# Kernel optimization log

Hardware: AMD Instinct MI355X
Metric: run time of the kernel (lower is better)

Reference implementation:

```python
import jax, jax.numpy as jnp
import numpy as np

D_MODEL = 1024
NHEAD = 16
HEAD_DIM = D_MODEL // NHEAD
B, L = 4, 4096
LN_EPS = 1e-5


def setup_inputs() -> dict:
    key = jax.random.key(0)
    ks = jax.random.split(key, 8)
    x = jax.random.normal(ks[0], (B, L, D_MODEL), dtype=jnp.float32)
    sin = jnp.zeros((L, HEAD_DIM), dtype=jnp.float32)
    cos = jnp.zeros((L, HEAD_DIM), dtype=jnp.float32)
    # decay[:,1,0] is read as per-head lambda in (0,1)
    decay = jax.random.uniform(ks[1], (NHEAD, 2, 1), dtype=jnp.float32)
    scale = 0.02
    Wq = jax.random.normal(ks[2], (D_MODEL, D_MODEL), dtype=jnp.float32) * scale
    Wv = jax.random.normal(ks[3], (D_MODEL, D_MODEL), dtype=jnp.float32) * scale
    Wo = jax.random.normal(ks[4], (D_MODEL, D_MODEL), dtype=jnp.float32) * scale
    Wg = jax.random.normal(ks[5], (D_MODEL, D_MODEL), dtype=jnp.float32) * scale
    ln_g = jnp.ones((D_MODEL,), dtype=jnp.float32)
    ln_b = jnp.zeros((D_MODEL,), dtype=jnp.float32)
    return {"x": x, "sin": sin, "cos": cos, "decay": decay,
            "Wq": Wq, "Wv": Wv, "Wo": Wo, "Wg": Wg,
            "ln_g": ln_g, "ln_b": ln_b}


def _retention(v, lam):
    # v: [B,L,H,Dh], lam: [H] -> cumulative decayed sum over L
    def step(state, v_t):  # state,[B,H,Dh]
        state = lam[None, :, None] * state + v_t
        return state, state
    v_l_first = jnp.swapaxes(v, 0, 1)  # [L,B,H,Dh]
    init = jnp.zeros(v_l_first.shape[1:], dtype=v.dtype)
    _, states = jax.lax.scan(step, init, v_l_first)
    return jnp.swapaxes(states, 0, 1)  # [B,L,H,Dh]


def reference(x, sin, cos, decay, Wq, Wv, Wo, Wg, ln_g, ln_b):
    del sin, cos  # discarded by the module
    Bx, Lx, D = x.shape
    H = decay.shape[0]
    Dh = D // H
    q = (x @ Wq.T).reshape(Bx, Lx, H, Dh)
    v = (x @ Wv.T).reshape(Bx, Lx, H, Dh)
    lam = decay[:, 1, 0]  # [H]
    state = _retention(v, lam)  # [B,L,H,Dh]
    y = (q * state).reshape(Bx, Lx, D)
    # LayerNorm over last dim
    mu = jnp.mean(y, axis=-1, keepdims=True)
    var = jnp.mean(jnp.square(y - mu), axis=-1, keepdims=True)
    y = (y - mu) * jax.lax.rsqrt(var + LN_EPS) * ln_g + ln_b
    gate = jax.nn.silu(x @ Wg.T)
    y = y * gate
    return y @ Wo.T
```

## Files before the change

### kernel.cpp

```cpp
#include <hip/hip_runtime.h>

#define DM    1024
#define LSEQ  4096
#define BATCH 4
#define MROWS (BATCH * LSEQ)
#define MD    ((size_t)MROWS * DM)
#define DD    ((size_t)DM * DM)
#define CHUNK 32
#define NCH   (LSEQ / CHUNK)
#define NCHAIN (BATCH * DM)

typedef __attribute__((ext_vector_type(4))) float  f32x4;
typedef __attribute__((ext_vector_type(8))) __bf16 bf16x8;
typedef __attribute__((ext_vector_type(4))) __bf16 bf16x4;

__device__ __forceinline__ void gload_lds16(const void* g, void* l) {
  __builtin_amdgcn_global_load_lds(
      (const __attribute__((address_space(1))) void*)g,
      (__attribute__((address_space(3))) void*)l, 16, 0, 0);
}

__global__ __launch_bounds__(256) void cvt_bf16(const float* __restrict__ in,
                                                __bf16* __restrict__ out) {
  size_t i = ((size_t)blockIdx.x * 256 + threadIdx.x) * 4;
  f32x4 f = *(const f32x4*)(in + i);
  bf16x4 o;
#pragma unroll
  for (int j = 0; j < 4; ++j) o[j] = (__bf16)f[j];
  *(bf16x4*)(out + i) = o;
}


__device__ __forceinline__ int swz(int b) { return b ^ ((b >> 3) & 0x70); }

__device__ __forceinline__ bf16x8 ldf(const char* tile, int row, int k) {
  int lin = (row << 7) + (k << 1);
  return *(const bf16x8*)(tile + swz(lin));
}

__device__ __forceinline__ void stage_half(const __bf16* srcRow0, char* tile,
                                           int halfOff, int k0, int t) {
#pragma unroll
  for (int is = 0; is < 2; ++is) {
    int d = halfOff + is * 8192 + t * 16;
    int l = swz(d);
    int row = l >> 7, cb = l & 127;
    gload_lds16((const char*)srcRow0 + (size_t)row * (DM * 2) + k0 * 2 + cb,
                tile + d);
  }
}

template <typename OutT>
__global__ __launch_bounds__(512, 2) void gemm_nt(const __bf16* __restrict__ A,
                                                  const __bf16* __restrict__ Wb,
                                                  OutT* __restrict__ Cb) {
  constexpr int K = DM, N = DM, NT = K / 64;
  __shared__ __attribute__((aligned(128))) char lds[131072];

  const __bf16* Wp = Wb + (size_t)blockIdx.z * DD;
  OutT* Cp = Cb + (size_t)blockIdx.z * MD;

  const int orig = blockIdx.y * 4 + blockIdx.x;
  const int sid = (orig & 7) * 32 + (orig >> 3);
  const int bx = sid & 3, by = sid >> 2;
  const int m0 = by * 256, n0 = bx * 256;

  const int t = threadIdx.x, lane = t & 63, wv = t >> 6;
  const int wr = wv >> 2, wc = wv & 3;
  const int lrow = lane & 15, lk8 = (lane >> 4) * 8;

  const __bf16* Abase = A + (size_t)m0 * K;
  const __bf16* Bbase = Wp + (size_t)n0 * K;

  f32x4 acc[8][4] = {};
  bf16x8 a[4][2];
  bf16x8 bq[2][2][2];

  char* buf0 = lds;
  char* buf1 = lds + 65536;

  stage_half(Abase, buf0,         0,  0, t);
  stage_half(Abase, buf0,     16384,  0, t);
  stage_half(Bbase, buf0 + 32768, 0,  0, t);
  stage_half(Bbase, buf0 + 32768, 16384, 0, t);
  stage_half(Bbase, buf1 + 32768, 0, 64, t);
  stage_half(Abase, buf1,         0, 64, t);
  asm volatile("s_waitcnt vmcnt(4)" ::: "memory");
  __builtin_amdgcn_s_barrier();
  __builtin_amdgcn_sched_barrier(0);

#define LDA_(mh)                                                        \
  _Pragma("unroll") for (int mf = 0; mf < 4; ++mf)                      \
  _Pragma("unroll") for (int ks = 0; ks < 2; ++ks)                      \
    a[mf][ks] = ldf(At, wr * 128 + (mh) * 64 + mf * 16 + lrow, ks * 32 + lk8);
#define LDB_(nh)                                                        \
  _Pragma("unroll") for (int nf = 0; nf < 2; ++nf)                      \
  _Pragma("unroll") for (int ks = 0; ks < 2; ++ks)                      \
    bq[nh][nf][ks] = ldf(Bt, wc * 64 + (nh) * 32 + nf * 16 + lrow, ks * 32 + lk8);
#define MFMA16_(mh, nh)                                                 \
  __builtin_amdgcn_s_setprio(1);                                        \
  _Pragma("unroll") for (int mf = 0; mf < 4; ++mf)                      \
  _Pragma("unroll") for (int nf = 0; nf < 2; ++nf)                      \
  _Pragma("unroll") for (int ks = 0; ks < 2; ++ks)                      \
    acc[(mh) * 4 + mf][(nh) * 2 + nf] = __builtin_amdgcn_mfma_f32_16x16x32_bf16( \
        a[mf][ks], bq[nh][nf][ks], acc[(mh) * 4 + mf][(nh) * 2 + nf], 0, 0, 0); \
  __builtin_amdgcn_s_setprio(0);
#define SYNC_IN_                                                        \
  __builtin_amdgcn_s_barrier();                                         \
  asm volatile("s_waitcnt lgkmcnt(0)" ::: "memory");                    \
  __builtin_amdgcn_sched_barrier(0);
#define SYNC_OUT_                                                       \
  __builtin_amdgcn_s_barrier();                                         \
  __builtin_amdgcn_sched_barrier(0);

#pragma unroll 1
  for (int kt = 0; kt < NT; ++kt) {
    char* bufc = lds + (kt & 1) * 65536;
    char* bufn = lds + (((kt & 1) ^ 1)) * 65536;
    const char* At = bufc;
    const char* Bt = bufc + 32768;
    const int k1 = (kt + 1) << 6, k2 = (kt + 2) << 6;
    const bool s1 = (kt + 1 < NT), s2 = (kt + 2 < NT);

    LDA_(0); LDB_(0);
    if (s1) stage_half(Bbase, bufn + 32768, 16384, k1, t);
    SYNC_IN_; MFMA16_(0, 0); SYNC_OUT_;

    LDB_(1);
    if (s1) stage_half(Abase, bufn, 16384, k1, t);
    SYNC_IN_; MFMA16_(0, 1); SYNC_OUT_;

    LDA_(1);
    if (s2) stage_half(Bbase, bufc + 32768, 0, k2, t);
    SYNC_IN_; MFMA16_(1, 0); SYNC_OUT_;

    if (s2) stage_half(Abase, bufc, 0, k2, t);
    __builtin_amdgcn_s_barrier();
    __builtin_amdgcn_sched_barrier(0);
    MFMA16_(1, 1);
    if (s2) { asm volatile("s_waitcnt vmcnt(4)" ::: "memory"); }
    else    { asm volatile("s_waitcnt vmcnt(0)" ::: "memory"); }
    __builtin_amdgcn_s_barrier();
    __builtin_amdgcn_sched_barrier(0);
  }
#undef LDA_
#undef LDB_
#undef MFMA16_
#undef SYNC_IN_
#undef SYNC_OUT_

#pragma unroll
  for (int mi = 0; mi < 8; ++mi) {
    int r0 = m0 + wr * 128 + mi * 16 + (lane >> 4) * 4;
#pragma unroll
    for (int ni = 0; ni < 4; ++ni) {
      int c0 = n0 + wc * 64 + ni * 16 + (lane & 15);
#pragma unroll
      for (int j = 0; j < 4; ++j) {
        float v = acc[mi][ni][j];
        if constexpr (__is_same(OutT, float))
          Cp[(size_t)(r0 + j) * N + c0] = v;
        else
          Cp[(size_t)(r0 + j) * N + c0] = (__bf16)v;
      }
    }
  }
}

__global__ __launch_bounds__(256) void scan1(const __bf16* __restrict__ v,
                                             float* __restrict__ st,
                                             float* __restrict__ csum,
                                             const float* __restrict__ decay) {
  int tid = blockIdx.x * 256 + threadIdx.x;
  int dg = tid & 255;
  int b  = (tid >> 8) & 3;
  int c  = tid >> 10;
  int d0 = dg * 4;
  float lam = decay[((d0 >> 6) << 1) + 1];
  f32x4 s = {0.f, 0.f, 0.f, 0.f};
  size_t base = ((size_t)b * LSEQ + (size_t)c * CHUNK) * DM + d0;
  for (int t = 0; t < CHUNK; ++t) {
    bf16x4 vv = *(const bf16x4*)(v + base);
    f32x4 vf = {(float)vv[0], (float)vv[1], (float)vv[2], (float)vv[3]};
    s = lam * s + vf;
    *(f32x4*)(st + base) = s;
    base += DM;
  }
  *(f32x4*)(csum + (size_t)c * NCHAIN + b * DM + d0) = s;
}

__global__ __launch_bounds__(256) void scan2(const float* __restrict__ csum,
                                             float* __restrict__ carry,
                                             const float* __restrict__ decay) {
  int i = blockIdx.x * 256 + threadIdx.x;
  int ch0 = i * 4;
  int d0 = ch0 & (DM - 1);
  float lam = decay[((d0 >> 6) << 1) + 1];
  float l2 = lam * lam, l4 = l2 * l2, l8 = l4 * l4, l16 = l8 * l8;
  float lamC = l16 * l16;
  f32x4 cs = {0.f, 0.f, 0.f, 0.f};
  for (int c = 0; c < NCH; ++c) {
    *(f32x4*)(carry + (size_t)c * NCHAIN + ch0) = cs;
    f32x4 sm = *(const f32x4*)(csum + (size_t)c * NCHAIN + ch0);
    cs = lamC * cs + sm;
  }
}

__global__ __launch_bounds__(256) void fuse_ln(const __bf16* __restrict__ qb,
                                               const float* __restrict__ st,
                                               const float* __restrict__ carry,
                                               const __bf16* __restrict__ gb,
                                               const float* __restrict__ decay,
                                               const float* __restrict__ ln_g,
                                               const float* __restrict__ ln_b,
                                               __bf16* __restrict__ y2) {
  const int row = blockIdx.x;
  const int l = row & (LSEQ - 1), b = row >> 12;
  const int c = l >> 5, tl = l & (CHUNK - 1);
  const int d0 = threadIdx.x * 4;
  const float lam = decay[((d0 >> 6) << 1) + 1];
  const float p = __powf(lam, (float)(tl + 1));
  const size_t base = (size_t)row * DM + d0;

  f32x4 s4 = *(const f32x4*)(st + base);
  f32x4 cr = *(const f32x4*)(carry + (size_t)c * NCHAIN + b * DM + d0);
  bf16x4 q4 = *(const bf16x4*)(qb + base);

  f32x4 y;
  float sum = 0.f, ssq = 0.f;
#pragma unroll
  for (int i = 0; i < 4; ++i) {
    float yy = (float)q4[i] * (s4[i] + p * cr[i]);
    y[i] = yy;
    sum += yy;
    ssq += yy * yy;
  }
#pragma unroll
  for (int o = 32; o > 0; o >>= 1) {
    sum += __shfl_xor(sum, o);
    ssq += __shfl_xor(ssq, o);
  }
  __shared__ float sb[8];
  if ((threadIdx.x & 63) == 0) {
    sb[threadIdx.x >> 6] = sum;
    sb[4 + (threadIdx.x >> 6)] = ssq;
  }
  __syncthreads();
  sum = sb[0] + sb[1] + sb[2] + sb[3];
  ssq = sb[4] + sb[5] + sb[6] + sb[7];

  const float mu = sum * (1.0f / DM);
  const float var = ssq * (1.0f / DM) - mu * mu;
  const float rstd = rsqrtf(fmaxf(var, 0.0f) + 1e-5f);

  bf16x4 g4 = *(const bf16x4*)(gb + base);
  f32x4 lg = *(const f32x4*)(ln_g + d0);
  f32x4 lb = *(const f32x4*)(ln_b + d0);
  bf16x4 o4;
#pragma unroll
  for (int i = 0; i < 4; ++i) {
    float gv = (float)g4[i];
    float gate = gv / (1.0f + __expf(-gv));
    float val = fmaf((y[i] - mu) * rstd, lg[i], lb[i]) * gate;
    o4[i] = (__bf16)val;
  }
  *(bf16x4*)(y2 + base) = o4;
}

extern "C" void kernel_launch(void* const* d_in, const int* in_sizes, int n_in,
                              void* d_out, int out_size, void* d_ws, size_t ws_size,
                              hipStream_t stream) {
  const float* x     = (const float*)d_in[0];
  const float* decay = (const float*)d_in[3];
  const float* Wq    = (const float*)d_in[4];
  const float* Wv    = (const float*)d_in[5];
  const float* Wo    = (const float*)d_in[6];
  const float* Wg    = (const float*)d_in[7];
  const float* lng   = (const float*)d_in[8];
  const float* lnb   = (const float*)d_in[9];
  float* out = (float*)d_out;

  char* ws = (char*)d_ws;
  size_t off = 0;
  auto alloc = [&](size_t bytes) -> void* {
    void* p = ws + off;
    off += (bytes + 255) & ~(size_t)255;
    return p;
  };
  __bf16* xb   = (__bf16*)alloc(MD * 2);
  __bf16* wqvg = (__bf16*)alloc(3 * DD * 2);
  __bf16* wob  = (__bf16*)alloc(DD * 2);
  __bf16* qvg  = (__bf16*)alloc(3 * MD * 2);
  __bf16* y2b  = (__bf16*)alloc(MD * 2);
  float*  st   = (float*)alloc(MD * 4);
  float*  csum = (float*)alloc((size_t)NCH * NCHAIN * 4);
  float*  cry  = (float*)alloc((size_t)NCH * NCHAIN * 4);

  cvt_bf16<<<(int)(MD / 1024), 256, 0, stream>>>(x, xb);
  cvt_bf16<<<(int)(DD / 1024), 256, 0, stream>>>(Wq, wqvg);
  cvt_bf16<<<(int)(DD / 1024), 256, 0, stream>>>(Wv, wqvg + DD);
  cvt_bf16<<<(int)(DD / 1024), 256, 0, stream>>>(Wg, wqvg + 2 * DD);
  cvt_bf16<<<(int)(DD / 1024), 256, 0, stream>>>(Wo, wob);

  gemm_nt<__bf16><<<dim3(4, MROWS / 256, 3), 512, 0, stream>>>(xb, wqvg, qvg);

  scan1<<<(BATCH * NCH * (DM / 4)) / 256, 256, 0, stream>>>(qvg + MD, st, csum, decay);
  scan2<<<(NCHAIN / 4) / 256, 256, 0, stream>>>(csum, cry, decay);

  fuse_ln<<<MROWS, 256, 0, stream>>>(qvg, st, cry, qvg + 2 * MD, decay, lng, lnb, y2b);

  gemm_nt<float><<<dim3(4, MROWS / 256, 1), 512, 0, stream>>>(y2b, wob, out);
}
```

Baseline: 235.4 us.

## Restructure GEMM staging pipeline, recompute scan in fused LN kernel, batch weight casts

The GEMM's global-to-LDS staging now remaps tile rows so that each half-tile matches what the MFMA phases consume. Loads for tile k+2 are issued into the current buffer with vmcnt-based waits, and the accumulator-to-output mapping is updated to match. The first scan pass no longer writes the full fp32 state tensor. A new per-chunk kernel instead recomputes the within-chunk scan from v plus the carry, then applies LayerNorm and the SiLU gate over 32 rows, which removes a large fp32 write and read. The four weight casts are merged into one launch. The costs are higher register pressure (32 f32x4 kept live per thread), only 512 blocks in the fused kernel, and a more fragile wait-count schedule.

Result: faster. 215.5 us (-8.5%).

```diff
diff --git a/kernel.cpp b/kernel.cpp
--- a/kernel.cpp
+++ b/kernel.cpp
@@ -30,6 +30,21 @@
   *(bf16x4*)(out + i) = o;
 }
 
+__global__ __launch_bounds__(256) void cvt_w(const float* __restrict__ s0,
+                                             const float* __restrict__ s1,
+                                             const float* __restrict__ s2,
+                                             const float* __restrict__ s3,
+                                             __bf16* __restrict__ dst) {
+  const float* sp = (blockIdx.z == 0) ? s0 : (blockIdx.z == 1) ? s1
+                  : (blockIdx.z == 2) ? s2 : s3;
+  size_t i = ((size_t)blockIdx.x * 256 + threadIdx.x) * 4;
+  f32x4 f = *(const f32x4*)(sp + i);
+  bf16x4 o;
+#pragma unroll
+  for (int j = 0; j < 4; ++j) o[j] = (__bf16)f[j];
+  *(bf16x4*)(dst + (size_t)blockIdx.z * DD + i) = o;
+}
+
 
 __device__ __forceinline__ int swz(int b) { return b ^ ((b >> 3) & 0x70); }
 
@@ -38,15 +53,26 @@
   return *(const bf16x8*)(tile + swz(lin));
 }
 
-__device__ __forceinline__ void stage_half(const __bf16* srcRow0, char* tile,
-                                           int halfOff, int k0, int t) {
+__device__ __forceinline__ void stageA_half(const __bf16* Abase, char* tileA,
+                                            int h, int k0, int t) {
 #pragma unroll
   for (int is = 0; is < 2; ++is) {
-    int d = halfOff + is * 8192 + t * 16;
+    int d = h * 16384 + is * 8192 + t * 16;
     int l = swz(d);
-    int row = l >> 7, cb = l & 127;
-    gload_lds16((const char*)srcRow0 + (size_t)row * (DM * 2) + k0 * 2 + cb,
-                tile + d);
+    int lds_r = l >> 7, cb = l & 127;
+    int g = ((lds_r >> 6) & 1) * 128 + h * 64 + (lds_r & 63);
+    gload_lds16((const char*)Abase + (size_t)g * (DM * 2) + k0 * 2 + cb, tileA + d);
+  }
+}
+__device__ __forceinline__ void stageB_half(const __bf16* Bbase, char* tileB,
+                                            int h, int k0, int t) {
+#pragma unroll
+  for (int is = 0; is < 2; ++is) {
+    int d = h * 16384 + is * 8192 + t * 16;
+    int l = swz(d);
+    int lds_r = l >> 7, cb = l & 127;
+    int g = ((lds_r >> 5) & 3) * 64 + h * 32 + (lds_r & 31);
+    gload_lds16((const char*)Bbase + (size_t)g * (DM * 2) + k0 * 2 + cb, tileB + d);
   }
 }
 
@@ -79,24 +105,26 @@
   char* buf0 = lds;
   char* buf1 = lds + 65536;
 
-  stage_half(Abase, buf0,         0,  0, t);
-  stage_half(Abase, buf0,     16384,  0, t);
-  stage_half(Bbase, buf0 + 32768, 0,  0, t);
-  stage_half(Bbase, buf0 + 32768, 16384, 0, t);
-  stage_half(Bbase, buf1 + 32768, 0, 64, t);
-  stage_half(Abase, buf1,         0, 64, t);
-  asm volatile("s_waitcnt vmcnt(4)" ::: "memory");
+  stageA_half(Abase, buf0,         0, 0, t);
+  stageB_half(Bbase, buf0 + 32768, 0, 0, t);
+  stageB_half(Bbase, buf0 + 32768, 1, 0, t);
+  stageA_half(Abase, buf0,         1, 0, t);
+  stageA_half(Abase, buf1,         0, 64, t);
+  stageB_half(Bbase, buf1 + 32768, 0, 64, t);
+  stageB_half(Bbase, buf1 + 32768, 1, 64, t);
+  stageA_half(Abase, buf1,         1, 64, t);
+  asm volatile("s_waitcnt vmcnt(12)" ::: "memory");
   __builtin_amdgcn_s_barrier();
   __builtin_amdgcn_sched_barrier(0);
 
 #define LDA_(mh)                                                        \
   _Pragma("unroll") for (int mf = 0; mf < 4; ++mf)                      \
   _Pragma("unroll") for (int ks = 0; ks < 2; ++ks)                      \
-    a[mf][ks] = ldf(At, wr * 128 + (mh) * 64 + mf * 16 + lrow, ks * 32 + lk8);
+    a[mf][ks] = ldf(At, (mh) * 128 + wr * 64 + mf * 16 + lrow, ks * 32 + lk8);
 #define LDB_(nh)                                                        \
   _Pragma("unroll") for (int nf = 0; nf < 2; ++nf)                      \
   _Pragma("unroll") for (int ks = 0; ks < 2; ++ks)                      \
-    bq[nh][nf][ks] = ldf(Bt, wc * 64 + (nh) * 32 + nf * 16 + lrow, ks * 32 + lk8);
+    bq[nh][nf][ks] = ldf(Bt, (nh) * 128 + wc * 32 + nf * 16 + lrow, ks * 32 + lk8);
 #define MFMA16_(mh, nh)                                                 \
   __builtin_amdgcn_s_setprio(1);                                        \
   _Pragma("unroll") for (int mf = 0; mf < 4; ++mf)                      \
@@ -105,56 +133,54 @@
     acc[(mh) * 4 + mf][(nh) * 2 + nf] = __builtin_amdgcn_mfma_f32_16x16x32_bf16( \
         a[mf][ks], bq[nh][nf][ks], acc[(mh) * 4 + mf][(nh) * 2 + nf], 0, 0, 0); \
   __builtin_amdgcn_s_setprio(0);
-#define SYNC_IN_                                                        \
+#define BAR_LGKM_                                                       \
   __builtin_amdgcn_s_barrier();                                         \
   asm volatile("s_waitcnt lgkmcnt(0)" ::: "memory");                    \
   __builtin_amdgcn_sched_barrier(0);
-#define SYNC_OUT_                                                       \
+#define VM_BAR_(n)                                                      \
+  asm volatile("s_waitcnt vmcnt(" #n ")" ::: "memory");                 \
   __builtin_amdgcn_s_barrier();                                         \
   __builtin_amdgcn_sched_barrier(0);
 
 #pragma unroll 1
   for (int kt = 0; kt < NT; ++kt) {
     char* bufc = lds + (kt & 1) * 65536;
-    char* bufn = lds + (((kt & 1) ^ 1)) * 65536;
     const char* At = bufc;
     const char* Bt = bufc + 32768;
-    const int k1 = (kt + 1) << 6, k2 = (kt + 2) << 6;
-    const bool s1 = (kt + 1 < NT), s2 = (kt + 2 < NT);
+    const int k2 = ((kt + 2) & (NT - 1)) << 6;
 
     LDA_(0); LDB_(0);
-    if (s1) stage_half(Bbase, bufn + 32768, 16384, k1, t);
-    SYNC_IN_; MFMA16_(0, 0); SYNC_OUT_;
+    BAR_LGKM_; MFMA16_(0, 0);
+    VM_BAR_(10);
 
     LDB_(1);
-    if (s1) stage_half(Abase, bufn, 16384, k1, t);
-    SYNC_IN_; MFMA16_(0, 1); SYNC_OUT_;
+    stageA_half(Abase, bufc,         0, k2, t);
+    stageB_half(Bbase, bufc + 32768, 0, k2, t);
+    BAR_LGKM_; MFMA16_(0, 1);
+    VM_BAR_(12);
 
     LDA_(1);
-    if (s2) stage_half(Bbase, bufc + 32768, 0, k2, t);
-    SYNC_IN_; MFMA16_(1, 0); SYNC_OUT_;
-
-    if (s2) stage_half(Abase, bufc, 0, k2, t);
+    stageB_half(Bbase, bufc + 32768, 1, k2, t);
+    BAR_LGKM_; MFMA16_(1, 0);
     __builtin_amdgcn_s_barrier();
     __builtin_amdgcn_sched_barrier(0);
+
+    stageA_half(Abase, bufc, 1, k2, t);
     MFMA16_(1, 1);
-    if (s2) { asm volatile("s_waitcnt vmcnt(4)" ::: "memory"); }
-    else    { asm volatile("s_waitcnt vmcnt(0)" ::: "memory"); }
-    __builtin_amdgcn_s_barrier();
-    __builtin_amdgcn_sched_barrier(0);
+    VM_BAR_(12);
   }
 #undef LDA_
 #undef LDB_
 #undef MFMA16_
-#undef SYNC_IN_
-#undef SYNC_OUT_
+#undef BAR_LGKM_
+#undef VM_BAR_
 
 #pragma unroll
   for (int mi = 0; mi < 8; ++mi) {
-    int r0 = m0 + wr * 128 + mi * 16 + (lane >> 4) * 4;
+    int r0 = m0 + wr * 128 + (mi >> 2) * 64 + (mi & 3) * 16 + (lane >> 4) * 4;
 #pragma unroll
     for (int ni = 0; ni < 4; ++ni) {
-      int c0 = n0 + wc * 64 + ni * 16 + (lane & 15);
+      int c0 = n0 + wc * 64 + (ni >> 1) * 32 + (ni & 1) * 16 + (lane & 15);
 #pragma unroll
       for (int j = 0; j < 4; ++j) {
         float v = acc[mi][ni][j];
@@ -167,10 +193,9 @@
   }
 }
 
-__global__ __launch_bounds__(256) void scan1(const __bf16* __restrict__ v,
-                                             float* __restrict__ st,
-                                             float* __restrict__ csum,
-                                             const float* __restrict__ decay) {
+__global__ __launch_bounds__(256) void scan_sum(const __bf16* __restrict__ v,
+                                                float* __restrict__ csum,
+                                                const float* __restrict__ decay) {
   int tid = blockIdx.x * 256 + threadIdx.x;
   int dg = tid & 255;
   int b  = (tid >> 8) & 3;
@@ -183,7 +208,6 @@
     bf16x4 vv = *(const bf16x4*)(v + base);
     f32x4 vf = {(float)vv[0], (float)vv[1], (float)vv[2], (float)vv[3]};
     s = lam * s + vf;
-    *(f32x4*)(st + base) = s;
     base += DM;
   }
   *(f32x4*)(csum + (size_t)c * NCHAIN + b * DM + d0) = s;
@@ -206,65 +230,72 @@
   }
 }
 
-__global__ __launch_bounds__(256) void fuse_ln(const __bf16* __restrict__ qb,
-                                               const float* __restrict__ st,
-                                               const float* __restrict__ carry,
-                                               const __bf16* __restrict__ gb,
-                                               const float* __restrict__ decay,
-                                               const float* __restrict__ ln_g,
-                                               const float* __restrict__ ln_b,
-                                               __bf16* __restrict__ y2) {
-  const int row = blockIdx.x;
-  const int l = row & (LSEQ - 1), b = row >> 12;
-  const int c = l >> 5, tl = l & (CHUNK - 1);
-  const int d0 = threadIdx.x * 4;
+__global__ __launch_bounds__(256) void fuse_chunk(
+    const __bf16* __restrict__ qb, const __bf16* __restrict__ vb,
+    const __bf16* __restrict__ gb, const float* __restrict__ carry,
+    const float* __restrict__ decay, const float* __restrict__ ln_g,
+    const float* __restrict__ ln_b, __bf16* __restrict__ y2) {
+  const int blk = blockIdx.x;
+  const int b = blk >> 7, c = blk & 127;
+  const int t = threadIdx.x, lane = t & 63, wv = t >> 6;
+  const int d0 = t * 4;
   const float lam = decay[((d0 >> 6) << 1) + 1];
-  const float p = __powf(lam, (float)(tl + 1));
-  const size_t base = (size_t)row * DM + d0;
-
-  f32x4 s4 = *(const f32x4*)(st + base);
-  f32x4 cr = *(const f32x4*)(carry + (size_t)c * NCHAIN + b * DM + d0);
-  bf16x4 q4 = *(const bf16x4*)(qb + base);
-
-  f32x4 y;
-  float sum = 0.f, ssq = 0.f;
-#pragma unroll
-  for (int i = 0; i < 4; ++i) {
-    float yy = (float)q4[i] * (s4[i] + p * cr[i]);
-    y[i] = yy;
-    sum += yy;
-    ssq += yy * yy;
-  }
-#pragma unroll
-  for (int o = 32; o > 0; o >>= 1) {
-    sum += __shfl_xor(sum, o);
-    ssq += __shfl_xor(ssq, o);
-  }
-  __shared__ float sb[8];
-  if ((threadIdx.x & 63) == 0) {
-    sb[threadIdx.x >> 6] = sum;
-    sb[4 + (threadIdx.x >> 6)] = ssq;
+  f32x4 s = *(const f32x4*)(carry + (size_t)c * NCHAIN + b * DM + d0);
+  const size_t base0 = ((size_t)b * LSEQ + (size_t)c * CHUNK) * DM + d0;
+
+  __shared__ float sbs[2][32][4];
+  __shared__ float stats[32][2];
+
+  f32x4 y[32];
+#pragma unroll
+  for (int r = 0; r < 32; ++r) {
+    size_t base = base0 + (size_t)r * DM;
+    bf16x4 v4 = *(const bf16x4*)(vb + base);
+    bf16x4 q4 = *(const bf16x4*)(qb + base);
+    f32x4 vf = {(float)v4[0], (float)v4[1], (float)v4[2], (float)v4[3]};
+    s = lam * s + vf;
+    f32x4 yy;
+    float su = 0.f, sq = 0.f;
+#pragma unroll
+    for (int i = 0; i < 4; ++i) {
+      float val = (float)q4[i] * s[i];
+      yy[i] = val; su += val; sq += val * val;
+    }
+    y[r] = yy;
+#pragma unroll
+    for (int o = 32; o > 0; o >>= 1) {
+      su += __shfl_xor(su, o);
+      sq += __shfl_xor(sq, o);
+    }
+    if (lane == 0) { sbs[0][r][wv] = su; sbs[1][r][wv] = sq; }
   }
   __syncthreads();
-  sum = sb[0] + sb[1] + sb[2] + sb[3];
-  ssq = sb[4] + sb[5] + sb[6] + sb[7];
-
-  const float mu = sum * (1.0f / DM);
-  const float var = ssq * (1.0f / DM) - mu * mu;
-  const float rstd = rsqrtf(fmaxf(var, 0.0f) + 1e-5f);
-
-  bf16x4 g4 = *(const bf16x4*)(gb + base);
+  if (t < 32) {
+    float su = sbs[0][t][0] + sbs[0][t][1] + sbs[0][t][2] + sbs[0][t][3];
+    float sq = sbs[1][t][0] + sbs[1][t][1] + sbs[1][t][2] + sbs[1][t][3];
+    float mu = su * (1.0f / DM);
+    float var = sq * (1.0f / DM) - mu * mu;
+    stats[t][0] = mu;
+    stats[t][1] = rsqrtf(fmaxf(var, 0.0f) + 1e-5f);
+  }
+  __syncthreads();
+
   f32x4 lg = *(const f32x4*)(ln_g + d0);
   f32x4 lb = *(const f32x4*)(ln_b + d0);
-  bf16x4 o4;
-#pragma unroll
-  for (int i = 0; i < 4; ++i) {
-    float gv = (float)g4[i];
-    float gate = gv / (1.0f + __expf(-gv));
-    float val = fmaf((y[i] - mu) * rstd, lg[i], lb[i]) * gate;
-    o4[i] = (__bf16)val;
-  }
-  *(bf16x4*)(y2 + base) = o4;
+#pragma unroll
+  for (int r = 0; r < 32; ++r) {
+    size_t base = base0 + (size_t)r * DM;
+    bf16x4 g4 = *(const bf16x4*)(gb + base);
+    const float mu = stats[r][0], rstd = stats[r][1];
+    bf16x4 o4;
+#pragma unroll
+    for (int i = 0; i < 4; ++i) {
+      float gv = (float)g4[i];
+      float gate = gv / (1.0f + __expf(-gv));
+      o4[i] = (__bf16)(fmaf((y[r][i] - mu) * rstd, lg[i], lb[i]) * gate);
+    }
+    *(bf16x4*)(y2 + base) = o4;
+  }
 }
 
 extern "C" void kernel_launch(void* const* d_in, const int* in_sizes, int n_in,
@@ -288,26 +319,22 @@
     return p;
   };
   __bf16* xb   = (__bf16*)alloc(MD * 2);
-  __bf16* wqvg = (__bf16*)alloc(3 * DD * 2);
-  __bf16* wob  = (__bf16*)alloc(DD * 2);
+  __bf16* w4   = (__bf16*)alloc(4 * DD * 2);
   __bf16* qvg  = (__bf16*)alloc(3 * MD * 2);
   __bf16* y2b  = (__bf16*)alloc(MD * 2);
-  float*  st   = (float*)alloc(MD * 4);
   float*  csum = (float*)alloc((size_t)NCH * NCHAIN * 4);
   float*  cry  = (float*)alloc((size_t)NCH * NCHAIN * 4);
 
   cvt_bf16<<<(int)(MD / 1024), 256, 0, stream>>>(x, xb);
-  cvt_bf16<<<(int)(DD / 1024), 256, 0, stream>>>(Wq, wqvg);
-  cvt_bf16<<<(int)(DD / 1024), 256, 0, stream>>>(Wv, wqvg + DD);
-  cvt_bf16<<<(int)(DD / 1024), 256, 0, stream>>>(Wg, wqvg + 2 * DD);
-  cvt_bf16<<<(int)(DD / 1024), 256, 0, stream>>>(Wo, wob);
-
-  gemm_nt<__bf16><<<dim3(4, MROWS / 256, 3), 512, 0, stream>>>(xb, wqvg, qvg);
-
-  scan1<<<(BATCH * NCH * (DM / 4)) / 256, 256, 0, stream>>>(qvg + MD, st, csum, decay);
+  cvt_w<<<dim3((unsigned)(DD / 1024), 1, 4), 256, 0, stream>>>(Wq, Wv, Wg, Wo, w4);
+
+  gemm_nt<__bf16><<<dim3(4, MROWS / 256, 3), 512, 0, stream>>>(xb, w4, qvg);
+
+  scan_sum<<<(BATCH * NCH * (DM / 4)) / 256, 256, 0, stream>>>(qvg + MD, csum, decay);
   scan2<<<(NCHAIN / 4) / 256, 256, 0, stream>>>(csum, cry, decay);
 
-  fuse_ln<<<MROWS, 256, 0, stream>>>(qvg, st, cry, qvg + 2 * MD, decay, lng, lnb, y2b);
-
-  gemm_nt<float><<<dim3(4, MROWS / 256, 1), 512, 0, stream>>>(y2b, wob, out);
-}
+  fuse_chunk<<<BATCH * NCH, 256, 0, stream>>>(qvg, qvg + MD, qvg + 2 * MD, cry,
+                                              decay, lng, lnb, y2b);
+
+  gemm_nt<float><<<dim3(4, MROWS / 256, 1), 512, 0, stream>>>(y2b, w4 + 3 * DD, out);
+}
```
